# Optimization experiments

Measured on AMD Instinct MI355X. Metric: run time of the kernel, lower is better.

## Reference

```python
import jax, jax.numpy as jnp
import numpy as np

HIDDEN = 1024
NUM_HEADS = 16
HEAD_DIM = HIDDEN // NUM_HEADS
ROPE_BASE = 10000.0
LN_EPS = 1e-8


def _rope_cos_sin(seq_len, dim, dtype=jnp.float32):
    inv_freq = 1.0 / (ROPE_BASE ** (jnp.arange(0, dim, 2, dtype=jnp.float32) / dim))
    t = jnp.arange(seq_len, dtype=jnp.float32)
    freqs = jnp.einsum('i,j->ij', t, inv_freq)          # [S, dim/2]
    emb = jnp.concatenate([freqs, freqs], axis=-1)       # [S, dim]
    return jnp.cos(emb).astype(dtype), jnp.sin(emb).astype(dtype)


def _rotate_half(x):
    x1, x2 = jnp.split(x, 2, axis=-1)
    return jnp.concatenate([-x2, x1], axis=-1)


def setup_inputs() -> dict:
    key = jax.random.key(0)
    ks = jax.random.split(key, 8)
    B, S, H = 4, 2048, HIDDEN
    x = jax.random.normal(ks[0], (B, S, H), dtype=jnp.float32)
    # causal mask, True = attend
    attn_mask = jnp.tril(jnp.ones((S, S), dtype=bool))[None].repeat(B, axis=0)
    lim_p = 1.0 / np.sqrt(H)
    Wp = jax.random.uniform(ks[1], (H, 4 * H), minval=-lim_p, maxval=lim_p, dtype=jnp.float32)
    bp = jax.random.uniform(ks[2], (4 * H,), minval=-lim_p, maxval=lim_p, dtype=jnp.float32)
    ln_g = jnp.ones((H,), dtype=jnp.float32)
    ln_b = jnp.zeros((H,), dtype=jnp.float32)
    Wt = jax.random.uniform(ks[3], (H, H), minval=-lim_p, maxval=lim_p, dtype=jnp.float32)
    bt = jax.random.uniform(ks[4], (H,), minval=-lim_p, maxval=lim_p, dtype=jnp.float32)
    return {"x": x, "attn_mask": attn_mask, "Wp": Wp, "bp": bp,
            "ln_g": ln_g, "ln_b": ln_b, "Wt": Wt, "bt": bt}


def reference(x, attn_mask, Wp, bp, ln_g, ln_b, Wt, bt):
    B, S, H = x.shape
    nh, hd = NUM_HEADS, HEAD_DIM
    proj = x @ Wp + bp                                   # [B,S,4H]
    U, V, Q, K = jnp.split(proj, 4, axis=-1)
    # [B, nh, S, hd]
    Q = Q.reshape(B, S, nh, hd).transpose(0, 2, 1, 3)
    K = K.reshape(B, S, nh, hd).transpose(0, 2, 1, 3)
    V = V.reshape(B, S, nh, hd).transpose(0, 2, 1, 3)
    cos, sin = _rope_cos_sin(S, hd, x.dtype)             # [S, hd]
    Qr = Q * cos + _rotate_half(Q) * sin
    Kr = K * cos + _rotate_half(K) * sin
    scale = hd ** -0.5
    scores = jnp.einsum('bhqd,bhkd->bhqk', Qr, Kr) * scale
    # masked positions -> sigmoid(-inf) == 0; use where for grad safety
    attn = jnp.where(attn_mask[:, None, :, :], jax.nn.sigmoid(scores), 0.0)
    attn_out = jnp.einsum('bhqk,bhkd->bhqd', attn, V)
    attn_out = attn_out.transpose(0, 2, 1, 3).reshape(B, S, H)
    mu = jnp.mean(attn_out, axis=-1, keepdims=True)
    var = jnp.var(attn_out, axis=-1, keepdims=True)
    attn_out = (attn_out - mu) / jnp.sqrt(var + LN_EPS) * ln_g + ln_b
    gated = jax.nn.silu(U) * attn_out
    out = gated @ Wt + bt
    return x + out
```

## Files before the change

### kernel.cpp

```cpp
#include <hip/hip_runtime.h>
#include <math.h>

#define H 1024
#define NH 16
#define HD 64
#define B_ 4
#define S_ 2048
#define ROWS (B_*S_)

#define QSCALE (-0.1803368801111664f)
#define ROPE_C (9.210340371976184f / 32.0f)

typedef __bf16 bf16x2_t __attribute__((ext_vector_type(2)));
typedef __bf16 bf16x4_t __attribute__((ext_vector_type(4)));
typedef __bf16 bf16x8_t __attribute__((ext_vector_type(8)));
typedef float floatx4_t __attribute__((ext_vector_type(4)));
typedef float floatx16_t __attribute__((ext_vector_type(16)));

#define GLOAD_LDS16(gp, lp)                                                        \
    __builtin_amdgcn_global_load_lds(                                              \
        (const __attribute__((address_space(1))) unsigned int*)(gp),               \
        (__attribute__((address_space(3))) unsigned int*)(lp), 16, 0, 0)

__global__ __launch_bounds__(256)
void prep_kernel(const float* __restrict__ x, const float* __restrict__ Wp,
                 const float* __restrict__ Wt,
                 __bf16* __restrict__ Ax, __bf16* __restrict__ Wp_t,
                 __bf16* __restrict__ Wt_t)
{
    __shared__ __bf16 t[32][33];
    const int flat = blockIdx.x;
    const int tid = threadIdx.x;

    if (flat < 8192) {
        size_t i = (size_t)flat * 256 + tid;
        float4 v = *reinterpret_cast<const float4*>(&x[i * 4]);
        bf16x4_t w = { (__bf16)v.x, (__bf16)v.y, (__bf16)v.z, (__bf16)v.w };
        *reinterpret_cast<bf16x4_t*>(&Ax[i * 4]) = w;
        return;
    }
    const float* W; __bf16* Wo; int K, N, bn, bk;
    if (flat < 12288) {
        int id = flat - 8192;  W = Wp; Wo = Wp_t; K = 1024; N = 4096;
        bn = (id & 127) * 32;  bk = (id >> 7) * 32;
    } else {
        int id = flat - 12288; W = Wt; Wo = Wt_t; K = 1024; N = 1024;
        bn = (id & 31) * 32;   bk = (id >> 5) * 32;
    }
    const int tx = tid & 31, ty = tid >> 5;
#pragma unroll
    for (int i = 0; i < 4; i++) {
        int r = ty + i * 8;
        t[tx][r] = (__bf16)W[(size_t)(bk + r) * N + bn + tx];
    }
    __syncthreads();
#pragma unroll
    for (int i = 0; i < 4; i++) {
        int r = ty + i * 8;
        Wo[(size_t)(bn + r) * K + bk + tx] = t[r][tx];
    }
}


#define MIN15(x) ((x) < 15 ? (x) : 15)

#define STAGE_A(buf, h, tile) do { int _kb = (tile) * 64 + (h) * 32;               \
        char* _lb = lwA + ((buf) * 2 + (h)) * 16384;                               \
        GLOAD_LDS16(a_src0 + _kb, _lb);                                            \
        GLOAD_LDS16(a_src1 + _kb, _lb + 1024); } while (0)
#define STAGE_B(buf, h, tile) do { int _kb = (tile) * 64 + (h) * 32;               \
        char* _lb = lwB + ((buf) * 2 + (h)) * 16384;                               \
        GLOAD_LDS16(b_src0 + _kb, _lb);                                            \
        GLOAD_LDS16(b_src1 + _kb, _lb + 1024); } while (0)

__global__ __launch_bounds__(512, 2)
void gemm_proj(const __bf16* __restrict__ A, const __bf16* __restrict__ Bt,
               const float* __restrict__ bias,
               __bf16* __restrict__ Ug, __bf16* __restrict__ Vh,
               __bf16* __restrict__ Qh, __bf16* __restrict__ Kh)
{
    __shared__ __attribute__((aligned(16))) char smem[131072];

    const int tid  = threadIdx.x;
    const int wave = tid >> 6, lane = tid & 63;
    const int ln15 = lane & 15, q4 = lane >> 4;
    const int wm = wave & 1, wn = wave >> 1;
    const int m0 = blockIdx.y * 256, n0 = blockIdx.x * 256;

    const int srow0 = wave * 32 + (lane >> 2);
    const int csrc  = (lane & 3) ^ ((lane >> 3) & 3);
    const __bf16* a_src0 = A  + (size_t)(m0 + srow0) * 1024 + csrc * 8;
    const __bf16* a_src1 = a_src0 + (size_t)16 * 1024;
    const __bf16* b_src0 = Bt + (size_t)(n0 + srow0) * 1024 + csrc * 8;
    const __bf16* b_src1 = b_src0 + (size_t)16 * 1024;
    char* lwA = smem + wave * 2048;
    char* lwB = smem + 65536 + wave * 2048;

    const int sl = (ln15 >> 1) & 3;
    const int a_lane = (wm * 128 + ln15) * 64 + ((q4 ^ sl) << 4);
    const int b_lane = (wn * 64  + ln15) * 64 + ((q4 ^ sl) << 4);

    floatx4_t acc[8][4];
#pragma unroll
    for (int i = 0; i < 8; i++)
#pragma unroll
        for (int j = 0; j < 4; j++) acc[i][j] = (floatx4_t){0.f, 0.f, 0.f, 0.f};

    STAGE_B(0, 0, 0); STAGE_A(0, 0, 0); STAGE_B(0, 1, 0); STAGE_A(0, 1, 0);
    STAGE_B(1, 0, 1); STAGE_A(1, 0, 1); STAGE_B(1, 1, 1);
    asm volatile("s_waitcnt vmcnt(6)" ::: "memory");
    __builtin_amdgcn_s_barrier();

    bf16x8_t bfr[4];

    for (int it = 0; it < 8; ++it) {
        const int T = 2 * it;
#pragma unroll
        for (int p = 0; p < 8; ++p) {
            const int buf = p >> 2, sub = p & 3, mh = sub & 1, kk = sub >> 1;
            const char* asl = smem + (buf * 2 + kk) * 16384;
            const char* bsl = smem + 65536 + (buf * 2 + kk) * 16384;

            if ((sub & 1) == 0) {
#pragma unroll
                for (int nf = 0; nf < 4; nf++)
                    bfr[nf] = *reinterpret_cast<const bf16x8_t*>(bsl + b_lane + nf * 1024);
            }
            bf16x8_t af[4];
#pragma unroll
            for (int mfi = 0; mfi < 4; mfi++)
                af[mfi] = *reinterpret_cast<const bf16x8_t*>(asl + a_lane + (mh * 4 + mfi) * 1024);

            if      (p == 0) STAGE_A(1, 1, MIN15(T + 1));
            else if (p == 1) STAGE_B(0, 0, MIN15(T + 2));
            else if (p == 2) STAGE_A(0, 0, MIN15(T + 2));
            else if (p == 3) STAGE_B(0, 1, MIN15(T + 2));
            else if (p == 4) STAGE_A(0, 1, MIN15(T + 2));
            else if (p == 5) STAGE_B(1, 0, MIN15(T + 3));
            else if (p == 6) STAGE_A(1, 0, MIN15(T + 3));
            else             STAGE_B(1, 1, MIN15(T + 3));

            if (p == 3 || p == 7)
                asm volatile("s_waitcnt vmcnt(6)" ::: "memory");
            __builtin_amdgcn_s_barrier();

            __builtin_amdgcn_s_setprio(1);
#pragma unroll
            for (int nf = 0; nf < 4; nf++)
#pragma unroll
                for (int mfi = 0; mfi < 4; mfi++)
                    acc[mh * 4 + mfi][nf] = __builtin_amdgcn_mfma_f32_16x16x32_bf16(
                        af[mfi], bfr[nf], acc[mh * 4 + mfi][nf], 0, 0, 0);
            __builtin_amdgcn_s_setprio(0);
            __builtin_amdgcn_s_barrier();
        }
    }
    asm volatile("s_waitcnt vmcnt(0)" ::: "memory");

    const int colbase = n0 + wn * 64;
    float bv[4];
#pragma unroll
    for (int nf = 0; nf < 4; nf++) bv[nf] = bias[colbase + nf * 16 + ln15];

    const int rowb = m0 + wm * 128 + q4 * 4;

    if (n0 < 1024) {
#pragma unroll
        for (int mf = 0; mf < 8; mf++)
#pragma unroll
            for (int nf = 0; nf < 4; nf++) {
                int col = colbase + nf * 16 + ln15;
#pragma unroll
                for (int reg = 0; reg < 4; reg++) {
                    int row = rowb + mf * 16 + reg;
                    Ug[(size_t)row * 1024 + col] = (__bf16)(acc[mf][nf][reg] + bv[nf]);
                }
            }
    } else if (n0 < 2048) {
        const int h = ((n0 - 1024) >> 6) + wn;
#pragma unroll
        for (int mf = 0; mf < 8; mf++)
#pragma unroll
            for (int reg = 0; reg < 4; reg++) {
                int row = rowb + mf * 16 + reg;
                int b = row >> 11, s = row & (S_ - 1);
                size_t orow = ((size_t)(b * NH + h) * S_ + s) * 64;
#pragma unroll
                for (int nf = 0; nf < 4; nf++)
                    Vh[orow + nf * 16 + ln15] = (__bf16)(acc[mf][nf][reg] + bv[nf]);
            }
    } else {
        const bool isQ = (n0 < 3072);
        const int h = ((n0 - (isQ ? 2048 : 3072)) >> 6) + wn;
        __bf16* dst = isQ ? Qh : Kh;
        const float sc = isQ ? QSCALE : 1.0f;
        float inv[2];
        inv[0] = __expf(-(float)(ln15)      * ROPE_C);
        inv[1] = __expf(-(float)(16 + ln15) * ROPE_C);
#pragma unroll
        for (int mf = 0; mf < 8; mf++)
#pragma unroll
            for (int reg = 0; reg < 4; reg++) {
                int row = rowb + mf * 16 + reg;
                int b = row >> 11, s = row & (S_ - 1);
                size_t orow = ((size_t)(b * NH + h) * S_ + s) * 64;
#pragma unroll
                for (int nf = 0; nf < 2; nf++) {
                    float sn, cs;
                    __sincosf((float)s * inv[nf], &sn, &cs);
                    float lo = acc[mf][nf][reg]     + bv[nf];
                    float hi = acc[mf][nf + 2][reg] + bv[nf + 2];
                    int d = nf * 16 + ln15;
                    dst[orow + d]      = (__bf16)((lo * cs - hi * sn) * sc);
                    dst[orow + 32 + d] = (__bf16)((hi * cs + lo * sn) * sc);
                }
            }
    }
}

__global__ __launch_bounds__(256)
void gemm_out(const __bf16* __restrict__ A, const __bf16* __restrict__ Bt,
              const float* __restrict__ bias, const float* __restrict__ resid,
              float* __restrict__ C, int M, int N, int K)
{
    __shared__ __bf16 As[128 * 32];
    __shared__ __bf16 Bs[128 * 32];

    const int tid  = threadIdx.x;
    const int wave = tid >> 6, lane = tid & 63;
    const int l31 = lane & 31, half = lane >> 5;
    const int wm = wave & 1, wn = wave >> 1;
    const int m0 = blockIdx.y * 128, n0 = blockIdx.x * 128;

    const int srow = lane >> 2;
    const int skc  = (((lane & 3) ^ ((srow >> 1) & 3)) * 8);

    const int fsw = (l31 >> 1) & 3;
    int aoff[2][2], boff[2][2];
#pragma unroll
    for (int mt = 0; mt < 2; mt++)
#pragma unroll
        for (int ks = 0; ks < 2; ks++) {
            int ra = wm * 64 + mt * 32 + l31;
            int rb = wn * 64 + mt * 32 + l31;
            int c = ks * 2 + half;
            aoff[mt][ks] = ra * 32 + ((c ^ fsw) * 8);
            boff[mt][ks] = rb * 32 + ((c ^ fsw) * 8);
        }

    floatx16_t acc[2][2];
#pragma unroll
    for (int i = 0; i < 2; i++)
#pragma unroll
        for (int j = 0; j < 2; j++) acc[i][j] = (floatx16_t)(0.f);

    for (int k0 = 0; k0 < K; k0 += 32) {
#pragma unroll
        for (int p = 0; p < 2; p++) {
            int i = wave * 2 + p;
            int rl = i * 16 + srow;
            GLOAD_LDS16(A  + (size_t)(m0 + rl) * K + k0 + skc, &As[i * 512]);
            GLOAD_LDS16(Bt + (size_t)(n0 + rl) * K + k0 + skc, &Bs[i * 512]);
        }
        __syncthreads();

        bf16x8_t af[2][2], bf[2][2];
#pragma unroll
        for (int mt = 0; mt < 2; mt++)
#pragma unroll
            for (int ks = 0; ks < 2; ks++) {
                af[mt][ks] = *reinterpret_cast<const bf16x8_t*>(&As[aoff[mt][ks]]);
                bf[mt][ks] = *reinterpret_cast<const bf16x8_t*>(&Bs[boff[mt][ks]]);
            }
#pragma unroll
        for (int ks = 0; ks < 2; ks++)
#pragma unroll
            for (int mt = 0; mt < 2; mt++)
#pragma unroll
                for (int nt = 0; nt < 2; nt++)
                    acc[mt][nt] = __builtin_amdgcn_mfma_f32_32x32x16_bf16(
                        af[mt][ks], bf[nt][ks], acc[mt][nt], 0, 0, 0);
        __syncthreads();
    }

#pragma unroll
    for (int mt = 0; mt < 2; mt++) {
#pragma unroll
        for (int nt = 0; nt < 2; nt++) {
            int col = n0 + wn * 64 + nt * 32 + l31;
            float bv = bias[col];
#pragma unroll
            for (int reg = 0; reg < 16; reg++) {
                int rowf = (reg & 3) + 8 * (reg >> 2) + 4 * half;
                int row = m0 + wm * 64 + mt * 32 + rowf;
                C[(size_t)row * N + col] = acc[mt][nt][reg] + bv + resid[(size_t)row * N + col];
            }
        }
    }
}

__global__ __launch_bounds__(256)
void transpose_v(const __bf16* __restrict__ Vh, __bf16* __restrict__ VtG)
{
    const int tid = threadIdx.x;
    const int st = blockIdx.x, bh = blockIdx.y;
    const int s0 = st * 64;
    const int d = tid & 63, k16 = tid >> 6;
    __bf16 vals[16];
#pragma unroll
    for (int j = 0; j < 16; j++) {
        int k = s0 + k16 * 16 + j;
        vals[j] = Vh[((size_t)bh * S_ + k) * 64 + d];
    }
    size_t orow = ((size_t)(bh * 64 + d)) * S_ + s0 + k16 * 16;
    *reinterpret_cast<bf16x8_t*>(&VtG[orow])     = *reinterpret_cast<bf16x8_t*>(&vals[0]);
    *reinterpret_cast<bf16x8_t*>(&VtG[orow + 8]) = *reinterpret_cast<bf16x8_t*>(&vals[8]);
}

__global__ __launch_bounds__(256)
void attn_mfma(const __bf16* __restrict__ Qh, const __bf16* __restrict__ Kh,
               const __bf16* __restrict__ VtG, __bf16* __restrict__ attn_out)
{
    __shared__ __bf16 Ks[2][4096];
    __shared__ __bf16 Vt[2][4096];
    __shared__ __bf16 Ps[4][16][72];

    const int tid = threadIdx.x, wave = tid >> 6, lane = tid & 63;
    const int quad = lane >> 4, ln = lane & 15;
    const int qt = (S_ / 128 - 1) - (blockIdx.x >> 6);
    const int hb = blockIdx.x & 63, h = hb & 15, b = hb >> 4, bh = b * NH + h;
    const int Q0 = qt * 128, T0 = 2 * qt;
    const int wl = wave * 16 + ln;

    const size_t qr = ((size_t)bh * S_ + Q0 + wl) * 64;
    bf16x8_t qa[2][2];
    qa[0][0] = *reinterpret_cast<const bf16x8_t*>(&Qh[qr + quad * 8]);
    qa[0][1] = *reinterpret_cast<const bf16x8_t*>(&Qh[qr + 32 + quad * 8]);
    qa[1][0] = *reinterpret_cast<const bf16x8_t*>(&Qh[qr + 4096 + quad * 8]);
    qa[1][1] = *reinterpret_cast<const bf16x8_t*>(&Qh[qr + 4096 + 32 + quad * 8]);

    const int sr = lane >> 3, scl = (lane & 7) ^ sr;
    const int c0 = wave * 2, c1 = c0 + 1;
    const size_t khead = (size_t)bh * S_ * 64;
    const int koff0 = (c0 * 8 + sr) * 64 + scl * 8;
    const int koff1 = (c1 * 8 + sr) * 64 + scl * 8;
    const size_t vg0 = ((size_t)bh * 64 + c0 * 8 + sr) * S_ + scl * 8;
    const size_t vg1 = ((size_t)bh * 64 + c1 * 8 + sr) * S_ + scl * 8;

    const int m7 = ln & 7;
    int ka[4][2];
#pragma unroll
    for (int nt = 0; nt < 4; nt++) {
        int row = nt * 16 + ln;
        ka[nt][0] = row * 64 + ((quad ^ m7) << 3);
        ka[nt][1] = row * 64 + (((quad + 4) ^ m7) << 3);
    }

    floatx4_t o[2][4];
#pragma unroll
    for (int s = 0; s < 2; s++)
#pragma unroll
        for (int dt = 0; dt < 4; dt++) o[s][dt] = (floatx4_t){0.f, 0.f, 0.f, 0.f};

    GLOAD_LDS16(Kh  + khead + koff0, &Ks[0][c0 * 512]);
    GLOAD_LDS16(Kh  + khead + koff1, &Ks[0][c1 * 512]);
    GLOAD_LDS16(VtG + vg0,           &Vt[0][c0 * 512]);
    GLOAD_LDS16(VtG + vg1,           &Vt[0][c1 * 512]);

    for (int kt = 0; kt <= T0 + 1; kt++) {
        const int buf = kt & 1;
        __syncthreads();
        if (kt <= T0) {
            const int nb = buf ^ 1;
            const size_t kg = khead + (size_t)(kt + 1) * 4096;
            GLOAD_LDS16(Kh  + kg + koff0,            &Ks[nb][c0 * 512]);
            GLOAD_LDS16(Kh  + kg + koff1,            &Ks[nb][c1 * 512]);
            GLOAD_LDS16(VtG + vg0 + (kt + 1) * 64,   &Vt[nb][c0 * 512]);
            GLOAD_LDS16(VtG + vg1 + (kt + 1) * 64,   &Vt[nb][c1 * 512]);
        }

        bf16x8_t kf[4][2], vf[4][2];
#pragma unroll
        for (int nt = 0; nt < 4; nt++) {
            kf[nt][0] = *reinterpret_cast<const bf16x8_t*>(&Ks[buf][ka[nt][0]]);
            kf[nt][1] = *reinterpret_cast<const bf16x8_t*>(&Ks[buf][ka[nt][1]]);
        }
#pragma unroll
        for (int dt = 0; dt < 4; dt++) {
            vf[dt][0] = *reinterpret_cast<const bf16x8_t*>(&Vt[buf][ka[dt][0]]);
            vf[dt][1] = *reinterpret_cast<const bf16x8_t*>(&Vt[buf][ka[dt][1]]);
        }

        const int mode0 = (kt < T0) ? 0 : ((kt == T0) ? 1 : 2);
        const int mode1 = (kt <= T0) ? 0 : 1;

#pragma unroll
        for (int s = 0; s < 2; s++) {
            const int mode = s ? mode1 : mode0;
            if (mode == 2) continue;

            floatx4_t st[4];
#pragma unroll
            for (int nt = 0; nt < 4; nt++) {
                floatx4_t acc = (floatx4_t){0.f, 0.f, 0.f, 0.f};
                acc = __builtin_amdgcn_mfma_f32_16x16x32_bf16(kf[nt][0], qa[s][0], acc, 0, 0, 0);
                acc = __builtin_amdgcn_mfma_f32_16x16x32_bf16(kf[nt][1], qa[s][1], acc, 0, 0, 0);
                st[nt] = acc;
            }

#pragma unroll
            for (int nt = 0; nt < 4; nt++) {
                bf16x4_t pk;
#pragma unroll
                for (int r = 0; r < 4; r++) {
                    float a = st[nt][r];
                    if (mode == 1) {
                        int kl = nt * 16 + quad * 4 + r;
                        a = (kl <= wl) ? a : __builtin_inff();
                    }
                    float p = __builtin_amdgcn_rcpf(1.f + __builtin_amdgcn_exp2f(a));
                    pk[r] = (__bf16)p;
                }
                *reinterpret_cast<bf16x4_t*>(&Ps[wave][ln][nt * 16 + quad * 4]) = pk;
            }

            const __bf16* prow = &Ps[wave][ln][quad * 8];
            bf16x8_t p0 = *reinterpret_cast<const bf16x8_t*>(prow);
            bf16x8_t p1 = *reinterpret_cast<const bf16x8_t*>(prow + 32);
#pragma unroll
            for (int dt = 0; dt < 4; dt++) {
                o[s][dt] = __builtin_amdgcn_mfma_f32_16x16x32_bf16(p0, vf[dt][0], o[s][dt], 0, 0, 0);
                o[s][dt] = __builtin_amdgcn_mfma_f32_16x16x32_bf16(p1, vf[dt][1], o[s][dt], 0, 0, 0);
            }
        }
    }

#pragma unroll
    for (int s = 0; s < 2; s++) {
        const int qrow_g = b * S_ + Q0 + s * 64 + wave * 16 + quad * 4;
#pragma unroll
        for (int dt = 0; dt < 4; dt++) {
#pragma unroll
            for (int reg = 0; reg < 4; reg++) {
                attn_out[(size_t)(qrow_g + reg) * H + h * 64 + dt * 16 + ln] =
                    (__bf16)o[s][dt][reg];
            }
        }
    }
}

__global__ __launch_bounds__(256)
void ln_gate_kernel(const __bf16* __restrict__ attn_out, const __bf16* __restrict__ Ug,
                    const float* __restrict__ ln_g, const float* __restrict__ ln_b,
                    __bf16* __restrict__ gated)
{
    const int row = blockIdx.x;
    const int tid = threadIdx.x;

    bf16x4_t vb = *reinterpret_cast<const bf16x4_t*>(&attn_out[(size_t)row * H + tid * 4]);
    float v0 = (float)vb[0], v1 = (float)vb[1], v2 = (float)vb[2], v3 = (float)vb[3];
    float s  = v0 + v1 + v2 + v3;
    float sq = v0 * v0 + v1 * v1 + v2 * v2 + v3 * v3;
#pragma unroll
    for (int off = 32; off > 0; off >>= 1) {
        s  += __shfl_down(s, off);
        sq += __shfl_down(sq, off);
    }
    __shared__ float ps[4], pq[4];
    int wave = tid >> 6, lane = tid & 63;
    if (lane == 0) { ps[wave] = s; pq[wave] = sq; }
    __syncthreads();
    float ts = ps[0] + ps[1] + ps[2] + ps[3];
    float tq = pq[0] + pq[1] + pq[2] + pq[3];
    float mu  = ts * (1.f / (float)H);
    float var = tq * (1.f / (float)H) - mu * mu;
    float rstd = rsqrtf(var + 1e-8f);

    bf16x4_t ub = *reinterpret_cast<const bf16x4_t*>(&Ug[(size_t)row * 1024 + tid * 4]);
    float4 g  = *reinterpret_cast<const float4*>(&ln_g[tid * 4]);
    float4 bb = *reinterpret_cast<const float4*>(&ln_b[tid * 4]);
    float u0 = (float)ub[0], u1 = (float)ub[1], u2 = (float)ub[2], u3 = (float)ub[3];
    bf16x4_t outv;
    outv[0] = (__bf16)(((v0 - mu) * rstd * g.x + bb.x) * (u0 / (1.f + __expf(-u0))));
    outv[1] = (__bf16)(((v1 - mu) * rstd * g.y + bb.y) * (u1 / (1.f + __expf(-u1))));
    outv[2] = (__bf16)(((v2 - mu) * rstd * g.z + bb.z) * (u2 / (1.f + __expf(-u2))));
    outv[3] = (__bf16)(((v3 - mu) * rstd * g.w + bb.w) * (u3 / (1.f + __expf(-u3))));
    *reinterpret_cast<bf16x4_t*>(&gated[(size_t)row * H + tid * 4]) = outv;
}

extern "C" void kernel_launch(void* const* d_in, const int* in_sizes, int n_in,
                              void* d_out, int out_size, void* d_ws, size_t ws_size,
                              hipStream_t stream)
{
    const float* x    = (const float*)d_in[0];
    const float* Wp   = (const float*)d_in[2];
    const float* bp   = (const float*)d_in[3];
    const float* ln_g = (const float*)d_in[4];
    const float* ln_b = (const float*)d_in[5];
    const float* Wt   = (const float*)d_in[6];
    const float* bt   = (const float*)d_in[7];
    float* out = (float*)d_out;

    char* ws = (char*)d_ws;
    const size_t MB = 1024 * 1024;
    __bf16* Ug    = (__bf16*)(ws);
    __bf16* Vh    = (__bf16*)(ws + 16  * MB);
    __bf16* Qh    = (__bf16*)(ws + 32  * MB);
    __bf16* Kh    = (__bf16*)(ws + 48  * MB);
    __bf16* attn  = (__bf16*)(ws + 64  * MB);
    __bf16* gated = (__bf16*)(ws + 80  * MB);
    __bf16* VtG   = (__bf16*)(ws + 96  * MB);
    __bf16* Ax    = (__bf16*)(ws + 112 * MB);
    __bf16* Wp_t  = (__bf16*)(ws + 128 * MB);
    __bf16* Wt_t  = (__bf16*)(ws + 136 * MB);

    prep_kernel<<<13312, 256, 0, stream>>>(x, Wp, Wt, Ax, Wp_t, Wt_t);

    dim3 g1(4096 / 256, ROWS / 256);
    gemm_proj<<<g1, 512, 0, stream>>>(Ax, Wp_t, bp, Ug, Vh, Qh, Kh);

    transpose_v<<<dim3(S_ / 64, B_ * NH), 256, 0, stream>>>(Vh, VtG);

    attn_mfma<<<(S_ / 128) * NH * B_, 256, 0, stream>>>(Qh, Kh, VtG, attn);

    ln_gate_kernel<<<ROWS, 256, 0, stream>>>(attn, Ug, ln_g, ln_b, gated);

    dim3 g3(1024 / 128, ROWS / 128);
    gemm_out<<<g3, 256, 0, stream>>>(gated, Wt_t, bt, x, out, ROWS, 1024, 1024);
}
```

Measured before the change: 341.0 us.

## Pair causal query tiles per 512-thread block for attention load balance

The attention kernel now launches 512-thread blocks with 8 waves, each wave owning one 16-row query slice. Each block processes two query tiles in sequence, tile 15-p and tile p, so every block does about the same amount of causal work. The grid halves, and each K/V tile loaded into LDS serves 128 query rows across 8 waves. In exchange, each wave now reads K/V fragments from LDS for only one query slice instead of two, so LDS traffic per unit of compute roughly doubles. The tighter launch bounds may also constrain registers.

```diff
diff --git a/kernel.cpp b/kernel.cpp
--- a/kernel.cpp
+++ b/kernel.cpp
@@ -317,35 +317,23 @@
     *reinterpret_cast<bf16x8_t*>(&VtG[orow + 8]) = *reinterpret_cast<bf16x8_t*>(&vals[8]);
 }
 
-__global__ __launch_bounds__(256)
+__global__ __launch_bounds__(512, 4)
 void attn_mfma(const __bf16* __restrict__ Qh, const __bf16* __restrict__ Kh,
                const __bf16* __restrict__ VtG, __bf16* __restrict__ attn_out)
 {
     __shared__ __bf16 Ks[2][4096];
     __shared__ __bf16 Vt[2][4096];
-    __shared__ __bf16 Ps[4][16][72];
+    __shared__ __bf16 Ps[8][16][72];
 
     const int tid = threadIdx.x, wave = tid >> 6, lane = tid & 63;
     const int quad = lane >> 4, ln = lane & 15;
-    const int qt = (S_ / 128 - 1) - (blockIdx.x >> 6);
+    const int p  = blockIdx.x >> 6;
     const int hb = blockIdx.x & 63, h = hb & 15, b = hb >> 4, bh = b * NH + h;
-    const int Q0 = qt * 128, T0 = 2 * qt;
-    const int wl = wave * 16 + ln;
-
-    const size_t qr = ((size_t)bh * S_ + Q0 + wl) * 64;
-    bf16x8_t qa[2][2];
-    qa[0][0] = *reinterpret_cast<const bf16x8_t*>(&Qh[qr + quad * 8]);
-    qa[0][1] = *reinterpret_cast<const bf16x8_t*>(&Qh[qr + 32 + quad * 8]);
-    qa[1][0] = *reinterpret_cast<const bf16x8_t*>(&Qh[qr + 4096 + quad * 8]);
-    qa[1][1] = *reinterpret_cast<const bf16x8_t*>(&Qh[qr + 4096 + 32 + quad * 8]);
 
     const int sr = lane >> 3, scl = (lane & 7) ^ sr;
-    const int c0 = wave * 2, c1 = c0 + 1;
     const size_t khead = (size_t)bh * S_ * 64;
-    const int koff0 = (c0 * 8 + sr) * 64 + scl * 8;
-    const int koff1 = (c1 * 8 + sr) * 64 + scl * 8;
-    const size_t vg0 = ((size_t)bh * 64 + c0 * 8 + sr) * S_ + scl * 8;
-    const size_t vg1 = ((size_t)bh * 64 + c1 * 8 + sr) * S_ + scl * 8;
+    const int koff = (wave * 8 + sr) * 64 + scl * 8;
+    const size_t vg = ((size_t)bh * 64 + wave * 8 + sr) * S_ + scl * 8;
 
     const int m7 = ln & 7;
     int ka[4][2];
@@ -356,55 +344,51 @@
         ka[nt][1] = row * 64 + (((quad + 4) ^ m7) << 3);
     }
 
-    floatx4_t o[2][4];
-#pragma unroll
-    for (int s = 0; s < 2; s++)
-#pragma unroll
-        for (int dt = 0; dt < 4; dt++) o[s][dt] = (floatx4_t){0.f, 0.f, 0.f, 0.f};
-
-    GLOAD_LDS16(Kh  + khead + koff0, &Ks[0][c0 * 512]);
-    GLOAD_LDS16(Kh  + khead + koff1, &Ks[0][c1 * 512]);
-    GLOAD_LDS16(VtG + vg0,           &Vt[0][c0 * 512]);
-    GLOAD_LDS16(VtG + vg1,           &Vt[0][c1 * 512]);
-
-    for (int kt = 0; kt <= T0 + 1; kt++) {
-        const int buf = kt & 1;
-        __syncthreads();
-        if (kt <= T0) {
-            const int nb = buf ^ 1;
-            const size_t kg = khead + (size_t)(kt + 1) * 4096;
-            GLOAD_LDS16(Kh  + kg + koff0,            &Ks[nb][c0 * 512]);
-            GLOAD_LDS16(Kh  + kg + koff1,            &Ks[nb][c1 * 512]);
-            GLOAD_LDS16(VtG + vg0 + (kt + 1) * 64,   &Vt[nb][c0 * 512]);
-            GLOAD_LDS16(VtG + vg1 + (kt + 1) * 64,   &Vt[nb][c1 * 512]);
-        }
-
-        bf16x8_t kf[4][2], vf[4][2];
-#pragma unroll
-        for (int nt = 0; nt < 4; nt++) {
-            kf[nt][0] = *reinterpret_cast<const bf16x8_t*>(&Ks[buf][ka[nt][0]]);
-            kf[nt][1] = *reinterpret_cast<const bf16x8_t*>(&Ks[buf][ka[nt][1]]);
-        }
-#pragma unroll
-        for (int dt = 0; dt < 4; dt++) {
-            vf[dt][0] = *reinterpret_cast<const bf16x8_t*>(&Vt[buf][ka[dt][0]]);
-            vf[dt][1] = *reinterpret_cast<const bf16x8_t*>(&Vt[buf][ka[dt][1]]);
-        }
-
-        const int mode0 = (kt < T0) ? 0 : ((kt == T0) ? 1 : 2);
-        const int mode1 = (kt <= T0) ? 0 : 1;
-
-#pragma unroll
-        for (int s = 0; s < 2; s++) {
-            const int mode = s ? mode1 : mode0;
+    const int wl   = wave * 16 + ln;
+    const int wl63 = wl & 63;
+    const bool hiw = wave >= 4;
+
+    for (int hf = 0; hf < 2; hf++) {
+        const int qt = hf ? p : (15 - p);
+        const int Q0 = qt * 128, T0 = 2 * qt;
+
+        const size_t qr = ((size_t)bh * S_ + Q0 + wl) * 64;
+        const bf16x8_t qa0 = *reinterpret_cast<const bf16x8_t*>(&Qh[qr + quad * 8]);
+        const bf16x8_t qa1 = *reinterpret_cast<const bf16x8_t*>(&Qh[qr + 32 + quad * 8]);
+
+        floatx4_t o[4];
+#pragma unroll
+        for (int dt = 0; dt < 4; dt++) o[dt] = (floatx4_t){0.f, 0.f, 0.f, 0.f};
+
+        GLOAD_LDS16(Kh  + khead + koff, &Ks[0][wave * 512]);
+        GLOAD_LDS16(VtG + vg,           &Vt[0][wave * 512]);
+
+        for (int kt = 0; kt <= T0 + 1; kt++) {
+            const int buf = kt & 1;
+            __syncthreads();
+            if (kt <= T0) {
+                const int nb = buf ^ 1;
+                GLOAD_LDS16(Kh  + khead + (size_t)(kt + 1) * 4096 + koff, &Ks[nb][wave * 512]);
+                GLOAD_LDS16(VtG + vg + (kt + 1) * 64,                      &Vt[nb][wave * 512]);
+            }
+
+            const int rel = kt - T0;
+            const int mode = (rel < 0) ? 0 : (rel == 0 ? (hiw ? 0 : 1) : (hiw ? 1 : 2));
             if (mode == 2) continue;
+
+            bf16x8_t kf[4][2];
+#pragma unroll
+            for (int nt = 0; nt < 4; nt++) {
+                kf[nt][0] = *reinterpret_cast<const bf16x8_t*>(&Ks[buf][ka[nt][0]]);
+                kf[nt][1] = *reinterpret_cast<const bf16x8_t*>(&Ks[buf][ka[nt][1]]);
+            }
 
             floatx4_t st[4];
 #pragma unroll
             for (int nt = 0; nt < 4; nt++) {
                 floatx4_t acc = (floatx4_t){0.f, 0.f, 0.f, 0.f};
-                acc = __builtin_amdgcn_mfma_f32_16x16x32_bf16(kf[nt][0], qa[s][0], acc, 0, 0, 0);
-                acc = __builtin_amdgcn_mfma_f32_16x16x32_bf16(kf[nt][1], qa[s][1], acc, 0, 0, 0);
+                acc = __builtin_amdgcn_mfma_f32_16x16x32_bf16(kf[nt][0], qa0, acc, 0, 0, 0);
+                acc = __builtin_amdgcn_mfma_f32_16x16x32_bf16(kf[nt][1], qa1, acc, 0, 0, 0);
                 st[nt] = acc;
             }
 
@@ -416,12 +400,19 @@
                     float a = st[nt][r];
                     if (mode == 1) {
                         int kl = nt * 16 + quad * 4 + r;
-                        a = (kl <= wl) ? a : __builtin_inff();
+                        a = (kl <= wl63) ? a : __builtin_inff();
                     }
-                    float p = __builtin_amdgcn_rcpf(1.f + __builtin_amdgcn_exp2f(a));
-                    pk[r] = (__bf16)p;
+                    float pv = __builtin_amdgcn_rcpf(1.f + __builtin_amdgcn_exp2f(a));
+                    pk[r] = (__bf16)pv;
                 }
                 *reinterpret_cast<bf16x4_t*>(&Ps[wave][ln][nt * 16 + quad * 4]) = pk;
+            }
+
+            bf16x8_t vf[4][2];
+#pragma unroll
+            for (int dt = 0; dt < 4; dt++) {
+                vf[dt][0] = *reinterpret_cast<const bf16x8_t*>(&Vt[buf][ka[dt][0]]);
+                vf[dt][1] = *reinterpret_cast<const bf16x8_t*>(&Vt[buf][ka[dt][1]]);
             }
 
             const __bf16* prow = &Ps[wave][ln][quad * 8];
@@ -429,21 +420,18 @@
             bf16x8_t p1 = *reinterpret_cast<const bf16x8_t*>(prow + 32);
 #pragma unroll
             for (int dt = 0; dt < 4; dt++) {
-                o[s][dt] = __builtin_amdgcn_mfma_f32_16x16x32_bf16(p0, vf[dt][0], o[s][dt], 0, 0, 0);
-                o[s][dt] = __builtin_amdgcn_mfma_f32_16x16x32_bf16(p1, vf[dt][1], o[s][dt], 0, 0, 0);
+                o[dt] = __builtin_amdgcn_mfma_f32_16x16x32_bf16(p0, vf[dt][0], o[dt], 0, 0, 0);
+                o[dt] = __builtin_amdgcn_mfma_f32_16x16x32_bf16(p1, vf[dt][1], o[dt], 0, 0, 0);
             }
         }
-    }
-
-#pragma unroll
-    for (int s = 0; s < 2; s++) {
-        const int qrow_g = b * S_ + Q0 + s * 64 + wave * 16 + quad * 4;
+
+        const int qrow_g = b * S_ + Q0 + wave * 16 + quad * 4;
 #pragma unroll
         for (int dt = 0; dt < 4; dt++) {
 #pragma unroll
             for (int reg = 0; reg < 4; reg++) {
                 attn_out[(size_t)(qrow_g + reg) * H + h * 64 + dt * 16 + ln] =
-                    (__bf16)o[s][dt][reg];
+                    (__bf16)o[dt][reg];
             }
         }
     }
@@ -521,7 +509,7 @@
 
     transpose_v<<<dim3(S_ / 64, B_ * NH), 256, 0, stream>>>(Vh, VtG);
 
-    attn_mfma<<<(S_ / 128) * NH * B_, 256, 0, stream>>>(Qh, Kh, VtG, attn);
+    attn_mfma<<<8 * B_ * NH, 512, 0, stream>>>(Qh, Kh, VtG, attn);
 
     ln_gate_kernel<<<ROWS, 256, 0, stream>>>(attn, Ug, ln_g, ln_b, gated);
 
```

Result: faster. 325.1 us (-4.6%).
